# Optimization experiments

Hardware: AMD Instinct MI355X
Metric: run time of the kernel (lower is better)

Reference implementation:

```python
import jax, jax.numpy as jnp
import numpy as np

N = 25000      # nodes per type
E = 300000     # weight-edge rows
K = 16         # neighbors
F = 64         # in_feat
A = 64         # atten_dim
DW = 64        # weight_dim
CB = 8         # num_bit_conv
CV = 8         # num_vector_conv
OUT = 64       # out_feat
IN_K = CB * F + CV * (3 + 2 + 1)


def setup_inputs() -> dict:
    key = jax.random.key(0)
    ks = jax.random.split(key, 40)
    s = 0.05
    d = {}
    d['eu'] = jax.random.normal(ks[0], (N, F), jnp.float32)
    d['ei'] = jax.random.normal(ks[1], (N, F), jnp.float32)
    d['et'] = jax.random.normal(ks[2], (N, F), jnp.float32)
    d['ew'] = jax.random.normal(ks[3], (E, DW), jnp.float32)
    names = ['u_iw_j', 'u_tw_j', 'i_uw_j', 'i_tw_j', 't_uw_j', 't_iw_j']
    for i, nm in enumerate(names):
        d[nm] = jax.random.randint(ks[4 + i], (N, K), 0, N, jnp.int64 if jax.config.jax_enable_x64 else jnp.int32)
        d[nm.replace('_j', '_w')] = jax.random.randint(ks[10 + i], (N, K), 0, E, jnp.int64 if jax.config.jax_enable_x64 else jnp.int32)
    # per-type Attention1 params: user, item, tag
    for i, t in enumerate(['user', 'item', 'tag']):
        b = 16 + 4 * i
        d[f'W1_{t}'] = jax.random.normal(ks[b], (F + DW, A), jnp.float32) * s
        d[f'W2_{t}'] = jax.random.normal(ks[b + 1], (F, A), jnp.float32) * s
        d[f'b_{t}'] = jax.random.normal(ks[b + 2], (1, A), jnp.float32) * s
        d[f'v_{t}'] = jax.random.normal(ks[b + 3], (1, A), jnp.float32) * s
    d['U'] = jax.random.normal(ks[28], (F, A), jnp.float32) * s
    d['q'] = jax.random.normal(ks[29], (1, A), jnp.float32) * s
    d['p'] = jax.random.normal(ks[30], (1, A), jnp.float32) * s
    d['W_bit'] = jax.random.normal(ks[31], (CB, 3), jnp.float32) * s       # Conv2d(1,CB,(3,1))
    d['W_vec1'] = jax.random.normal(ks[32], (CV, 1, F), jnp.float32) * s   # Conv2d(1,CV,(1,F))
    d['W_vec2'] = jax.random.normal(ks[33], (CV, 2, F), jnp.float32) * s
    d['W_vec3'] = jax.random.normal(ks[34], (CV, 3, F), jnp.float32) * s
    d['Wf'] = jax.random.normal(ks[35], (IN_K, OUT), jnp.float32) * s
    d['bf'] = jax.random.normal(ks[36], (1, OUT), jnp.float32) * s
    return d


def _atten1(ev, ej, ew, v_j, v_w, W1, W2, b, v):
    ejp = jnp.concatenate([jnp.zeros((1, ej.shape[1]), ej.dtype), ej], axis=0)
    ewp = jnp.concatenate([jnp.zeros((1, ew.shape[1]), ew.dtype), ew], axis=0)
    eNj = ejp[v_j]                                  # [N,K,F]
    eNw = ewp[v_w]                                  # [N,K,DW]
    eNv = jnp.broadcast_to(ev[:, None, :], (ev.shape[0], v_j.shape[1], ev.shape[1]))
    eN_vw = jnp.concatenate([eNv, eNw], axis=-1)    # [N,K,F+DW]
    av = jnp.einsum('nkd,da->nka', eN_vw, W1) + jnp.einsum('nkf,fa->nka', eNj, W2) + b
    x = jax.nn.relu(av) @ v.T                       # [N,K,1]
    a = jax.nn.softmax(x, axis=1)
    return jnp.sum(a * eNj, axis=1)                 # [N,F]


def _atten2(u, i, t, U, q, p):
    uit = jnp.stack([u, i, t], axis=1)              # [N,3,F]
    x = jnp.einsum('nsf,fa->nsa', uit, U) + q
    x = jax.nn.relu(x) @ p.T                        # [N,3,1]
    b = jax.nn.softmax(x, axis=1)
    return b * uit                                  # [N,3,F]


def _conv(eN, W_bit, W_vec1, W_vec2, W_vec3):
    # eN: [N,3,F]
    bit = jax.nn.relu(jnp.einsum('njf,cj->ncf', eN, W_bit))       # [N,CB,F]
    bit = bit.reshape(bit.shape[0], -1)
    vec = []
    for j, W in ((1, W_vec1), (2, W_vec2), (3, W_vec3)):
        win = jnp.stack([eN[:, s:s + j, :] for s in range(3 - j + 1)], axis=1)  # [N,4-j,j,F]
        y = jax.nn.relu(jnp.einsum('nsjf,cjf->ncs', win, W))       # [N,CV,4-j]
        vec.append(y.reshape(y.shape[0], -1))
    return jnp.concatenate([bit] + vec, axis=1)                    # [N,IN_K]


def _forward(eu, ei, et, ew, params, idx):
    (W1u, W2u, bu, vu, W1i, W2i, bi, vi, W1t, W2t, bt, vt,
     U, q, p, W_bit, W_vec1, W_vec2, W_vec3, Wf, bf) = params
    (u_iw_j, u_iw_w, u_tw_j, u_tw_w, i_uw_j, i_uw_w,
     i_tw_j, i_tw_w, t_uw_j, t_uw_w, t_iw_j, t_iw_w) = idx
    eu_iN = _atten1(eu, ei, ew, u_iw_j, u_iw_w, W1i, W2i, bi, vi)
    eu_tN = _atten1(eu, et, ew, u_tw_j, u_tw_w, W1t, W2t, bt, vt)
    ei_uN = _atten1(ei, eu, ew, i_uw_j, i_uw_w, W1u, W2u, bu, vu)
    ei_tN = _atten1(ei, et, ew, i_tw_j, i_tw_w, W1t, W2t, bt, vt)
    et_uN = _atten1(et, eu, ew, t_uw_j, t_uw_w, W1u, W2u, bu, vu)
    et_iN = _atten1(et, ei, ew, t_iw_j, t_iw_w, W1i, W2i, bi, vi)
    euN = _atten2(eu, eu_iN, eu_tN, U, q, p)
    eiN = _atten2(ei_uN, ei, ei_tN, U, q, p)
    etN = _atten2(et_uN, et_iN, et, U, q, p)
    out = []
    for eN in (euN, eiN, etN):
        c = _conv(eN, W_bit, W_vec1, W_vec2, W_vec3)
        out.append(jax.nn.relu(c @ Wf + bf))
    return tuple(out)


def reference(eu, ei, et, ew,
              u_iw_j, u_iw_w, u_tw_j, u_tw_w, i_uw_j, i_uw_w, i_tw_j, i_tw_w,
              t_uw_j, t_uw_w, t_iw_j, t_iw_w,
              W1_user, W2_user, b_user, v_user,
              W1_item, W2_item, b_item, v_item,
              W1_tag, W2_tag, b_tag, v_tag,
              U, q, p, W_bit, W_vec1, W_vec2, W_vec3, Wf, bf):
    params = (W1_user, W2_user, b_user, v_user, W1_item, W2_item, b_item, v_item,
              W1_tag, W2_tag, b_tag, v_tag, U, q, p, W_bit, W_vec1, W_vec2, W_vec3, Wf, bf)
    idx = (u_iw_j, u_iw_w, u_tw_j, u_tw_w, i_uw_j, i_uw_w,
           i_tw_j, i_tw_w, t_uw_j, t_uw_w, t_iw_j, t_iw_w)
    return _forward(eu, ei, et, ew, params, idx)
```

## Files before the change

### kernel.cpp

```cpp
#include <hip/hip_runtime.h>
#include <math.h>

#define NN 25000
#define EE 300000
#define NT 1563
#define NT64 391
#define ET64 4688

typedef __attribute__((ext_vector_type(8))) short bf16x8;
typedef __attribute__((ext_vector_type(4))) float f32x4;
typedef __attribute__((ext_vector_type(2))) float f32x2;

__device__ __forceinline__ unsigned short f2bf(float f) {
    union { float f; unsigned u; } a; a.f = f;
    unsigned r = (a.u + 0x7fffu + ((a.u >> 16) & 1u)) >> 16;
    return (unsigned short)r;
}
__device__ __forceinline__ unsigned pack2(float lo, float hi) {
    return (unsigned)f2bf(lo) | ((unsigned)f2bf(hi) << 16);
}
__device__ __forceinline__ float bflo(unsigned p) {
    union { unsigned u; float f; } a; a.u = p << 16; return a.f;
}
__device__ __forceinline__ float bfhi(unsigned p) {
    union { unsigned u; float f; } a; a.u = p & 0xffff0000u; return a.f;
}
__device__ __forceinline__ unsigned packfp8x4(float a, float b, float c, float d) {
    int v = __builtin_amdgcn_cvt_pk_fp8_f32(a, b, 0, 0);
    v = __builtin_amdgcn_cvt_pk_fp8_f32(c, d, v, 1);
    return (unsigned)v;
}

__global__ __launch_bounds__(256) void head_kernel(
    const float* __restrict__ ew,
    const float* __restrict__ eu, const float* __restrict__ ei, const float* __restrict__ et,
    const float* __restrict__ W1u, const float* __restrict__ W1i, const float* __restrict__ W1t,
    const float* __restrict__ W2u, const float* __restrict__ W2i, const float* __restrict__ W2t,
    const float* __restrict__ bu, const float* __restrict__ bi, const float* __restrict__ bt,
    unsigned char* __restrict__ gw8, unsigned* __restrict__ preB,
    unsigned char* __restrict__ JG)
{
    __shared__ __align__(16) unsigned short stA[64 * 72];
    __shared__ __align__(16) float cS[64 * 68];
    const int t = threadIdx.x;
    const int lane = t & 63, wv = t >> 6;
    const int l15 = lane & 15, quad = lane >> 4;
    const int cw = wv * 16 + l15;
    const int bx = blockIdx.x;

    if (bx < ET64) {
        if (bx == 0 && t < 48) {
            int w = t >> 4;
            ((unsigned*)(gw8 + (size_t)w * (EE + 1) * 64))[t & 15] = 0u;
        }
        const float* Ws[3] = { W1u + 4096, W1i + 4096, W1t + 4096 };
        bf16x8 bf[3][2];
        #pragma unroll
        for (int w = 0; w < 3; ++w)
            #pragma unroll
            for (int ks = 0; ks < 2; ++ks)
                #pragma unroll
                for (int j = 0; j < 8; ++j)
                    bf[w][ks][j] = (short)f2bf(Ws[w][(ks * 32 + quad * 8 + j) * 64 + cw]);

        const int rowBase = bx * 64;
        #pragma unroll
        for (int i = 0; i < 4; ++i) {
            int idx = t + i * 256;
            int row = idx >> 4, cg = idx & 15;
            int gr = rowBase + row;
            float4 v4 = (gr < EE) ? *(const float4*)(ew + (size_t)gr * 64 + cg * 4)
                                  : make_float4(0.f, 0.f, 0.f, 0.f);
            uint2 pk = { pack2(v4.x, v4.y), pack2(v4.z, v4.w) };
            *(uint2*)&stA[row * 72 + cg * 4] = pk;
        }
        __syncthreads();
        bf16x8 af[4][2];
        #pragma unroll
        for (int m = 0; m < 4; ++m)
            #pragma unroll
            for (int ks = 0; ks < 2; ++ks)
                af[m][ks] = *(const bf16x8*)&stA[(m * 16 + l15) * 72 + ks * 32 + quad * 8];

        #pragma unroll
        for (int w = 0; w < 3; ++w) {
            if (w) __syncthreads();
            f32x4 acc[4];
            #pragma unroll
            for (int m = 0; m < 4; ++m) {
                acc[m].x = 0; acc[m].y = 0; acc[m].z = 0; acc[m].w = 0;
                #pragma unroll
                for (int ks = 0; ks < 2; ++ks)
                    acc[m] = __builtin_amdgcn_mfma_f32_16x16x32_bf16(af[m][ks], bf[w][ks], acc[m], 0, 0, 0);
                #pragma unroll
                for (int r = 0; r < 4; ++r)
                    cS[(m * 16 + quad * 4 + r) * 68 + cw] = acc[m][r];
            }
            __syncthreads();
            unsigned char* outg = gw8 + (size_t)w * (EE + 1) * 64 + 64;
            #pragma unroll
            for (int i = 0; i < 2; ++i) {
                int task = t + i * 256;
                int row = task >> 3, seg = task & 7;
                int gr = rowBase + row;
                if (gr < EE) {
                    float4 a = *(const float4*)&cS[row * 68 + seg * 8];
                    float4 b = *(const float4*)&cS[row * 68 + seg * 8 + 4];
                    uint2 pk = { packfp8x4(a.x, a.y, a.z, a.w),
                                 packfp8x4(b.x, b.y, b.z, b.w) };
                    *(uint2*)(outg + (size_t)gr * 64 + seg * 8) = pk;
                }
            }
        }
    } else {
        const int yy = bx - ET64;
        const int y = yy / NT64;
        const int rowBase = (yy - y * NT64) * 64;
        if (rowBase == 0 && t < 48)
            ((unsigned*)(JG + (size_t)y * (NN + 1) * 192))[t] = 0u;
        const float* X; const float* Wa; const float* Wb; const float* W2;
        const float* ba; const float* bb; int oa, ob;
        switch (y) {
            case 0:  X = eu; Wa = W1i; ba = bi; oa = 0; Wb = W1t; bb = bt; ob = 1; W2 = W2u; break;
            case 1:  X = ei; Wa = W1u; ba = bu; oa = 2; Wb = W1t; bb = bt; ob = 3; W2 = W2i; break;
            default: X = et; Wa = W1u; ba = bu; oa = 4; Wb = W1i; bb = bi; ob = 5; W2 = W2t; break;
        }
        const float* Ws[3] = { Wa, Wb, W2 };
        const float bias_cw[3] = { ba[cw], bb[cw], 0.f };
        bf16x8 bf[3][2];
        #pragma unroll
        for (int w = 0; w < 3; ++w)
            #pragma unroll
            for (int ks = 0; ks < 2; ++ks)
                #pragma unroll
                for (int j = 0; j < 8; ++j)
                    bf[w][ks][j] = (short)f2bf(Ws[w][(ks * 32 + quad * 8 + j) * 64 + cw]);

        #pragma unroll
        for (int i = 0; i < 4; ++i) {
            int idx = t + i * 256;
            int row = idx >> 4, cg = idx & 15;
            int gr = rowBase + row;
            float4 v4 = (gr < NN) ? *(const float4*)(X + (size_t)gr * 64 + cg * 4)
                                  : make_float4(0.f, 0.f, 0.f, 0.f);
            uint2 pk = { pack2(v4.x, v4.y), pack2(v4.z, v4.w) };
            *(uint2*)&stA[row * 72 + cg * 4] = pk;
        }
        __syncthreads();
        bf16x8 af[4][2];
        #pragma unroll
        for (int m = 0; m < 4; ++m)
            #pragma unroll
            for (int ks = 0; ks < 2; ++ks)
                af[m][ks] = *(const bf16x8*)&stA[(m * 16 + l15) * 72 + ks * 32 + quad * 8];

        #pragma unroll
        for (int w = 0; w < 3; ++w) {
            if (w) __syncthreads();
            f32x4 acc[4];
            #pragma unroll
            for (int m = 0; m < 4; ++m) {
                acc[m].x = 0; acc[m].y = 0; acc[m].z = 0; acc[m].w = 0;
                #pragma unroll
                for (int ks = 0; ks < 2; ++ks)
                    acc[m] = __builtin_amdgcn_mfma_f32_16x16x32_bf16(af[m][ks], bf[w][ks], acc[m], 0, 0, 0);
                #pragma unroll
                for (int r = 0; r < 4; ++r)
                    cS[(m * 16 + quad * 4 + r) * 68 + cw] = acc[m][r] + bias_cw[w];
            }
            __syncthreads();
            #pragma unroll
            for (int i = 0; i < 2; ++i) {
                int task = t + i * 256;
                int row = task >> 3, seg = task & 7;
                int gr = rowBase + row;
                if (gr >= NN) continue;
                float4 a = *(const float4*)&cS[row * 68 + seg * 8];
                float4 b = *(const float4*)&cS[row * 68 + seg * 8 + 4];
                if (w < 2) {
                    int oi = (w == 0) ? oa : ob;
                    uint4 pk = { pack2(a.x, a.y), pack2(a.z, a.w),
                                 pack2(b.x, b.y), pack2(b.z, b.w) };
                    *(uint4*)(preB + ((size_t)oi * NN + gr) * 32 + seg * 4) = pk;
                } else {
                    unsigned char* dst = JG + ((size_t)y * (NN + 1) + gr + 1) * 192;
                    uint2 gj = { packfp8x4(a.x, a.y, a.z, a.w),
                                 packfp8x4(b.x, b.y, b.z, b.w) };
                    *(uint2*)(dst + seg * 8) = gj;
                    uint4 ej = *(const uint4*)&stA[row * 72 + seg * 8];
                    *(uint4*)(dst + 64 + seg * 16) = ej;
                }
            }
        }
    }
}

__global__ __launch_bounds__(256) void atten1_kernel(
    const unsigned* __restrict__ preB, const unsigned char* __restrict__ gw8,
    const unsigned char* __restrict__ JG,
    const float* __restrict__ vu, const float* __restrict__ vi, const float* __restrict__ vt,
    const int* __restrict__ u_iw_j, const int* __restrict__ u_iw_w,
    const int* __restrict__ u_tw_j, const int* __restrict__ u_tw_w,
    const int* __restrict__ i_uw_j, const int* __restrict__ i_uw_w,
    const int* __restrict__ i_tw_j, const int* __restrict__ i_tw_w,
    const int* __restrict__ t_uw_j, const int* __restrict__ t_uw_w,
    const int* __restrict__ t_iw_j, const int* __restrict__ t_iw_w,
    unsigned* __restrict__ aoB)
{
    const int y = blockIdx.y;
    const int* Vj; const int* Vw; const float* v; int g;
    switch (y) {
        case 0:  Vj = u_iw_j; Vw = u_iw_w; v = vi; g = 1; break;
        case 1:  Vj = u_tw_j; Vw = u_tw_w; v = vt; g = 2; break;
        case 2:  Vj = i_uw_j; Vw = i_uw_w; v = vu; g = 0; break;
        case 3:  Vj = i_tw_j; Vw = i_tw_w; v = vt; g = 2; break;
        case 4:  Vj = t_uw_j; Vw = t_uw_w; v = vu; g = 0; break;
        default: Vj = t_iw_j; Vw = t_iw_w; v = vi; g = 1; break;
    }
    const unsigned* pre = preB + (size_t)y * NN * 32;
    const unsigned char* gw = gw8 + (size_t)g * (EE + 1) * 64;
    const unsigned char* jg = JG + (size_t)g * (NN + 1) * 192;
    unsigned*            out = aoB + (size_t)y * NN * 32;

    const int lane = threadIdx.x & 63;
    const int n = blockIdx.x * 4 + (threadIdx.x >> 6);
    const int q = lane >> 4, r = lane & 15;

    const uint2 prep = *(const uint2*)(pre + (size_t)n * 32 + 2 * r);
    const float pf0 = bflo(prep.x), pf1 = bfhi(prep.x);
    const float pf2 = bflo(prep.y), pf3 = bfhi(prep.y);
    const float4 v4 = *(const float4*)(v + r * 4);

    const int4 wi = *(const int4*)(Vw + n * 16 + q * 4);
    const int4 ji = *(const int4*)(Vj + n * 16 + q * 4);
    const int wid[4] = { wi.x, wi.y, wi.z, wi.w };
    const int jid[4] = { ji.x, ji.y, ji.z, ji.w };

    unsigned gwv[4], gjv[4]; uint2 ejv[4];
    #pragma unroll
    for (int i = 0; i < 4; ++i)
        gwv[i] = *(const unsigned*)(gw + (size_t)wid[i] * 64 + r * 4);
    #pragma unroll
    for (int i = 0; i < 4; ++i) {
        const unsigned char* row = jg + (size_t)jid[i] * 192;
        gjv[i] = *(const unsigned*)(row + r * 4);
        ejv[i] = *(const uint2*)(row + 64 + r * 8);
    }

    float xk[4];
    #pragma unroll
    for (int i = 0; i < 4; ++i) {
        f32x2 g01 = __builtin_amdgcn_cvt_pk_f32_fp8((int)gwv[i], false);
        f32x2 g23 = __builtin_amdgcn_cvt_pk_f32_fp8((int)gwv[i], true);
        f32x2 j01 = __builtin_amdgcn_cvt_pk_f32_fp8((int)gjv[i], false);
        f32x2 j23 = __builtin_amdgcn_cvt_pk_f32_fp8((int)gjv[i], true);
        float x =          fmaxf(pf0 + g01.x + j01.x, 0.f) * v4.x;
        x = fmaf(fmaxf(pf1 + g01.y + j01.y, 0.f), v4.y, x);
        x = fmaf(fmaxf(pf2 + g23.x + j23.x, 0.f), v4.z, x);
        x = fmaf(fmaxf(pf3 + g23.y + j23.y, 0.f), v4.w, x);
        x += __shfl_xor(x, 1, 64);
        x += __shfl_xor(x, 2, 64);
        x += __shfl_xor(x, 4, 64);
        x += __shfl_xor(x, 8, 64);
        xk[i] = x;
    }
    float m = fmaxf(fmaxf(xk[0], xk[1]), fmaxf(xk[2], xk[3]));
    m = fmaxf(m, __shfl_xor(m, 16, 64));
    m = fmaxf(m, __shfl_xor(m, 32, 64));
    float e0 = __expf(xk[0] - m), e1 = __expf(xk[1] - m);
    float e2 = __expf(xk[2] - m), e3 = __expf(xk[3] - m);
    float s = (e0 + e1) + (e2 + e3);
    s += __shfl_xor(s, 16, 64);
    s += __shfl_xor(s, 32, 64);
    const float inv = 1.f / s;

    float a0 = 0.f, a1 = 0.f, a2 = 0.f, a3 = 0.f;
    const float wgt[4] = { e0 * inv, e1 * inv, e2 * inv, e3 * inv };
    #pragma unroll
    for (int i = 0; i < 4; ++i) {
        a0 = fmaf(wgt[i], bflo(ejv[i].x), a0);
        a1 = fmaf(wgt[i], bfhi(ejv[i].x), a1);
        a2 = fmaf(wgt[i], bflo(ejv[i].y), a2);
        a3 = fmaf(wgt[i], bfhi(ejv[i].y), a3);
    }
    a0 += __shfl_xor(a0, 16, 64); a0 += __shfl_xor(a0, 32, 64);
    a1 += __shfl_xor(a1, 16, 64); a1 += __shfl_xor(a1, 32, 64);
    a2 += __shfl_xor(a2, 16, 64); a2 += __shfl_xor(a2, 32, 64);
    a3 += __shfl_xor(a3, 16, 64); a3 += __shfl_xor(a3, 32, 64);
    if (q == 0) {
        uint2 pk = { pack2(a0, a1), pack2(a2, a3) };
        *(uint2*)(out + (size_t)n * 32 + 2 * r) = pk;
    }
}

__global__ __launch_bounds__(256, 3) void tail_kernel(
    const float* __restrict__ eu, const float* __restrict__ ei, const float* __restrict__ et,
    const unsigned* __restrict__ aoB,
    const float* __restrict__ U, const float* __restrict__ q, const float* __restrict__ p,
    const float* __restrict__ Wbit, const float* __restrict__ Wv1,
    const float* __restrict__ Wv2, const float* __restrict__ Wv3,
    const float* __restrict__ Wf, const float* __restrict__ bfv,
    float* __restrict__ out)
{
    __shared__ __align__(16) unsigned short uitA[48 * 72];
    __shared__ __align__(16) unsigned short eNA[48 * 72];
    __shared__ __align__(16) unsigned short wcf[6 * 64 * 8];
    __shared__ __align__(16) unsigned short c_sh[16 * 584];
    __shared__ float G_sh[48 * 52];
    __shared__ float xpart[4 * 48];
    __shared__ float bcoef[16 * 4];

    const int t = threadIdx.x;
    const int lane = t & 63;
    const int wv = t >> 6;
    const int l15 = lane & 15;
    const int quad = lane >> 4;
    const int type = blockIdx.y;
    const float* xf = (type == 0) ? eu : (type == 1) ? ei : et;
    const int cw = wv * 16 + l15;
    const float qv = q[cw], pv = p[cw], bfb = bfv[cw];

    float wb[8][3];
    #pragma unroll
    for (int c = 0; c < 8; ++c)
        #pragma unroll
        for (int s = 0; s < 3; ++s) wb[c][s] = Wbit[c * 3 + s];

    bf16x8 ufrag[2];
    #pragma unroll
    for (int ks = 0; ks < 2; ++ks)
        #pragma unroll
        for (int j = 0; j < 8; ++j) {
            int f = ks * 32 + quad * 8 + j;
            ufrag[ks][j] = (short)f2bf(U[f * 64 + cw]);
        }
    bf16x8 wff[18];
    #pragma unroll
    for (int ks = 0; ks < 18; ++ks)
        #pragma unroll
        for (int j = 0; j < 8; ++j) {
            int k = ks * 32 + quad * 8 + j;
            float w = (k < 560) ? Wf[(size_t)k * 64 + cw] : 0.f;
            wff[ks][j] = (short)f2bf(w);
        }
    for (int slot = t; slot < 384; slot += 256) {
        int fi = slot >> 6, l = slot & 63;
        int nt_ = fi >> 1, ks = fi & 1;
        int r = nt_ * 16 + (l & 15);
        unsigned short vals[8];
        #pragma unroll
        for (int j = 0; j < 8; ++j) {
            int f = ks * 32 + (l >> 4) * 8 + j;
            float wv_;
            if (r < 8)       wv_ = Wv1[r * 64 + f];
            else if (r < 24) { int u = r - 8;  wv_ = Wv2[(u >> 1) * 128 + (u & 1) * 64 + f]; }
            else             { int u = r - 24; wv_ = Wv3[(u / 3) * 192 + (u % 3) * 64 + f]; }
            vals[j] = f2bf(wv_);
        }
        uint4 pk = { (unsigned)vals[0] | ((unsigned)vals[1] << 16),
                     (unsigned)vals[2] | ((unsigned)vals[3] << 16),
                     (unsigned)vals[4] | ((unsigned)vals[5] << 16),
                     (unsigned)vals[6] | ((unsigned)vals[7] << 16) };
        *(uint4*)&wcf[slot * 8] = pk;
    }

    for (int tile = blockIdx.x; tile < NT; tile += gridDim.x) {
        const int nodeBase = tile * 16;
        __syncthreads();
        #pragma unroll
        for (int i = 0; i < 3; ++i) {
            int idx = t + i * 256;
            int row = idx >> 4, cg = idx & 15;
            int nl = row / 3, s = row - nl * 3;
            int n = nodeBase + nl;
            uint2 pk;
            if (s == type) {
                float4 v4 = (n < NN) ? *(const float4*)(xf + (size_t)n * 64 + cg * 4)
                                     : make_float4(0.f, 0.f, 0.f, 0.f);
                pk.x = pack2(v4.x, v4.y); pk.y = pack2(v4.z, v4.w);
            } else {
                int aoidx = (type == 0) ? (s - 1)
                          : (type == 1) ? ((s == 0) ? 2 : 3)
                                        : ((s == 0) ? 4 : 5);
                pk = (n < NN) ? *(const uint2*)(aoB + ((size_t)aoidx * NN + n) * 32 + cg * 2)
                              : make_uint2(0u, 0u);
            }
            *(uint2*)&uitA[row * 72 + cg * 4] = pk;
        }
        __syncthreads();
        {
            f32x4 av[3];
            #pragma unroll
            for (int mt = 0; mt < 3; ++mt) { av[mt].x = 0; av[mt].y = 0; av[mt].z = 0; av[mt].w = 0; }
            #pragma unroll
            for (int mt = 0; mt < 3; ++mt)
                #pragma unroll
                for (int ks = 0; ks < 2; ++ks) {
                    bf16x8 a = *(const bf16x8*)&uitA[(mt * 16 + l15) * 72 + ks * 32 + quad * 8];
                    av[mt] = __builtin_amdgcn_mfma_f32_16x16x32_bf16(a, ufrag[ks], av[mt], 0, 0, 0);
                }
            #pragma unroll
            for (int mt = 0; mt < 3; ++mt)
                #pragma unroll
                for (int r = 0; r < 4; ++r) {
                    float val = fmaxf(av[mt][r] + qv, 0.f) * pv;
                    val += __shfl_xor(val, 1, 64); val += __shfl_xor(val, 2, 64);
                    val += __shfl_xor(val, 4, 64); val += __shfl_xor(val, 8, 64);
                    if (l15 == 0) xpart[wv * 48 + mt * 16 + quad * 4 + r] = val;
                }
        }
        __syncthreads();
        if (t < 16) {
            float xv[3];
            #pragma unroll
            for (int s = 0; s < 3; ++s)
                xv[s] = xpart[t * 3 + s] + xpart[48 + t * 3 + s]
                      + xpart[96 + t * 3 + s] + xpart[144 + t * 3 + s];
            float mm = fmaxf(xv[0], fmaxf(xv[1], xv[2]));
            float e0 = __expf(xv[0] - mm), e1 = __expf(xv[1] - mm), e2 = __expf(xv[2] - mm);
            float inv = 1.f / (e0 + e1 + e2);
            bcoef[t * 4 + 0] = e0 * inv; bcoef[t * 4 + 1] = e1 * inv; bcoef[t * 4 + 2] = e2 * inv;
        }
        __syncthreads();
        #pragma unroll
        for (int i = 0; i < 2; ++i) {
            int task = t + i * 256;
            int nl = task >> 5, fp = task & 31;
            float b0 = bcoef[nl * 4], b1 = bcoef[nl * 4 + 1], b2 = bcoef[nl * 4 + 2];
            unsigned u0 = *(const unsigned*)&uitA[(nl * 3 + 0) * 72 + fp * 2];
            unsigned u1 = *(const unsigned*)&uitA[(nl * 3 + 1) * 72 + fp * 2];
            unsigned u2 = *(const unsigned*)&uitA[(nl * 3 + 2) * 72 + fp * 2];
            float e0l = b0 * bflo(u0), e0h = b0 * bfhi(u0);
            float e1l = b1 * bflo(u1), e1h = b1 * bfhi(u1);
            float e2l = b2 * bflo(u2), e2h = b2 * bfhi(u2);
            *(unsigned*)&eNA[(nl * 3 + 0) * 72 + fp * 2] = pack2(e0l, e0h);
            *(unsigned*)&eNA[(nl * 3 + 1) * 72 + fp * 2] = pack2(e1l, e1h);
            *(unsigned*)&eNA[(nl * 3 + 2) * 72 + fp * 2] = pack2(e2l, e2h);
            #pragma unroll
            for (int c = 0; c < 8; ++c) {
                float lo = fmaxf(wb[c][0] * e0l + wb[c][1] * e1l + wb[c][2] * e2l, 0.f);
                float hi = fmaxf(wb[c][0] * e0h + wb[c][1] * e1h + wb[c][2] * e2h, 0.f);
                *(unsigned*)&c_sh[nl * 584 + c * 64 + fp * 2] = pack2(lo, hi);
            }
        }
        __syncthreads();
        #pragma unroll
        for (int pi = 0; pi < 3; ++pi) {
            int pr = wv + pi * 4;
            if (pr < 9) {
                int mm = pr / 3, nn_ = pr - mm * 3;
                f32x4 g; g.x = 0; g.y = 0; g.z = 0; g.w = 0;
                #pragma unroll
                for (int ks = 0; ks < 2; ++ks) {
                    bf16x8 a = *(const bf16x8*)&eNA[(mm * 16 + l15) * 72 + ks * 32 + quad * 8];
                    bf16x8 b = *(const bf16x8*)&wcf[((nn_ * 2 + ks) * 64 + lane) * 8];
                    g = __builtin_amdgcn_mfma_f32_16x16x32_bf16(a, b, g, 0, 0, 0);
                }
                #pragma unroll
                for (int r = 0; r < 4; ++r)
                    G_sh[(mm * 16 + quad * 4 + r) * 52 + nn_ * 16 + l15] = g[r];
            }
        }
        __syncthreads();
        #pragma unroll
        for (int i = 0; i < 4; ++i) {
            int task = t + i * 256;
            int vvv = task >> 4, nl = task & 15;
            unsigned short res = 0;
            if (vvv < 24) {
                int c = vvv / 3, s = vvv - c * 3;
                res = f2bf(fmaxf(G_sh[(nl * 3 + s) * 52 + c], 0.f));
            } else if (vvv < 40) {
                int u = vvv - 24, c = u >> 1, s = u & 1;
                float val = G_sh[(nl * 3 + s) * 52 + 8 + 2 * c]
                          + G_sh[(nl * 3 + s + 1) * 52 + 8 + 2 * c + 1];
                res = f2bf(fmaxf(val, 0.f));
            } else if (vvv < 48) {
                int c = vvv - 40;
                float val = G_sh[(nl * 3 + 0) * 52 + 24 + 3 * c]
                          + G_sh[(nl * 3 + 1) * 52 + 24 + 3 * c + 1]
                          + G_sh[(nl * 3 + 2) * 52 + 24 + 3 * c + 2];
                res = f2bf(fmaxf(val, 0.f));
            }
            c_sh[nl * 584 + 512 + vvv] = res;
        }
        __syncthreads();
        {
            f32x4 acc; acc.x = 0; acc.y = 0; acc.z = 0; acc.w = 0;
            const unsigned short* ap = &c_sh[l15 * 584 + quad * 8];
            #pragma unroll
            for (int ks = 0; ks < 18; ++ks) {
                bf16x8 a = *(const bf16x8*)(ap + ks * 32);
                acc = __builtin_amdgcn_mfma_f32_16x16x32_bf16(a, wff[ks], acc, 0, 0, 0);
            }
            float* outT = out + (size_t)type * NN * 64;
            #pragma unroll
            for (int r = 0; r < 4; ++r) {
                int node = nodeBase + quad * 4 + r;
                if (node < NN) outT[(size_t)node * 64 + cw] = fmaxf(acc[r] + bfb, 0.f);
            }
        }
    }
}

extern "C" void kernel_launch(void* const* d_in, const int* in_sizes, int n_in,
                              void* d_out, int out_size, void* d_ws, size_t ws_size,
                              hipStream_t stream)
{
    const float* eu = (const float*)d_in[0];
    const float* ei = (const float*)d_in[1];
    const float* et = (const float*)d_in[2];
    const float* ew = (const float*)d_in[3];
    const int* u_iw_j = (const int*)d_in[4];
    const int* u_iw_w = (const int*)d_in[5];
    const int* u_tw_j = (const int*)d_in[6];
    const int* u_tw_w = (const int*)d_in[7];
    const int* i_uw_j = (const int*)d_in[8];
    const int* i_uw_w = (const int*)d_in[9];
    const int* i_tw_j = (const int*)d_in[10];
    const int* i_tw_w = (const int*)d_in[11];
    const int* t_uw_j = (const int*)d_in[12];
    const int* t_uw_w = (const int*)d_in[13];
    const int* t_iw_j = (const int*)d_in[14];
    const int* t_iw_w = (const int*)d_in[15];
    const float* W1_user = (const float*)d_in[16];
    const float* W2_user = (const float*)d_in[17];
    const float* b_user  = (const float*)d_in[18];
    const float* v_user  = (const float*)d_in[19];
    const float* W1_item = (const float*)d_in[20];
    const float* W2_item = (const float*)d_in[21];
    const float* b_item  = (const float*)d_in[22];
    const float* v_item  = (const float*)d_in[23];
    const float* W1_tag  = (const float*)d_in[24];
    const float* W2_tag  = (const float*)d_in[25];
    const float* b_tag   = (const float*)d_in[26];
    const float* v_tag   = (const float*)d_in[27];
    const float* U    = (const float*)d_in[28];
    const float* q    = (const float*)d_in[29];
    const float* p    = (const float*)d_in[30];
    const float* Wbit = (const float*)d_in[31];
    const float* Wv1  = (const float*)d_in[32];
    const float* Wv2  = (const float*)d_in[33];
    const float* Wv3  = (const float*)d_in[34];
    const float* Wf   = (const float*)d_in[35];
    const float* bfv  = (const float*)d_in[36];
    float* out = (float*)d_out;

    unsigned char* gw8 = (unsigned char*)d_ws;
    unsigned* preB = (unsigned*)(gw8 + (size_t)3 * (EE + 1) * 64);
    unsigned char* JG = (unsigned char*)(preB + (size_t)6 * NN * 32);
    unsigned* aoB = (unsigned*)(JG + (size_t)3 * (NN + 1) * 192);

    const dim3 blk(256);

    head_kernel<<<ET64 + 3 * NT64, blk, 0, stream>>>(
        ew, eu, ei, et,
        W1_user, W1_item, W1_tag, W2_user, W2_item, W2_tag,
        b_user, b_item, b_tag, gw8, preB, JG);

    atten1_kernel<<<dim3(NN / 4, 6), blk, 0, stream>>>(
        preB, gw8, JG, v_user, v_item, v_tag,
        u_iw_j, u_iw_w, u_tw_j, u_tw_w, i_uw_j, i_uw_w,
        i_tw_j, i_tw_w, t_uw_j, t_uw_w, t_iw_j, t_iw_w, aoB);

    tail_kernel<<<dim3(256, 3), blk, 0, stream>>>(
        eu, ei, et, aoB,
        U, q, p, Wbit, Wv1, Wv2, Wv3, Wf, bfv, out);
}
```

Before: 401.0 us.

## Use packed fp16 math in atten1 scoring and group blocks by gather table

The preB projection is now stored as fp16 instead of bf16. The atten1 score computation converts fp8 directly to packed half, adds and relus in packed fp16, and accumulates with fdot2 instead of scalar fp32 FMAs. The launch grid is also reordered so that adjacent blocks gather from the same embedding/weight table (by type g), which is meant to improve L2 locality for the random gathers. fp16 accumulation of the sums adds some precision risk.

```diff
diff --git a/kernel.cpp b/kernel.cpp
--- a/kernel.cpp
+++ b/kernel.cpp
@@ -10,6 +10,7 @@
 typedef __attribute__((ext_vector_type(8))) short bf16x8;
 typedef __attribute__((ext_vector_type(4))) float f32x4;
 typedef __attribute__((ext_vector_type(2))) float f32x2;
+typedef __attribute__((ext_vector_type(2))) __fp16 h2;
 
 __device__ __forceinline__ unsigned short f2bf(float f) {
     union { float f; unsigned u; } a; a.f = f;
@@ -29,6 +30,37 @@
     int v = __builtin_amdgcn_cvt_pk_fp8_f32(a, b, 0, 0);
     v = __builtin_amdgcn_cvt_pk_fp8_f32(c, d, v, 1);
     return (unsigned)v;
+}
+__device__ __forceinline__ unsigned pkh(float lo, float hi) {
+    h2 r = __builtin_amdgcn_cvt_pkrtz(lo, hi);
+    return __builtin_bit_cast(unsigned, r);
+}
+template<bool HI>
+__device__ __forceinline__ h2 fp8toh(unsigned v) {
+#if __has_builtin(__builtin_amdgcn_cvt_scalef32_pk_f16_fp8)
+    return __builtin_amdgcn_cvt_scalef32_pk_f16_fp8((int)v, 1.0f, HI);
+#else
+    f32x2 f = __builtin_amdgcn_cvt_pk_f32_fp8((int)v, HI);
+    return __builtin_amdgcn_cvt_pkrtz(f.x, f.y);
+#endif
+}
+__device__ __forceinline__ float hdot(h2 a, h2 b, float c) {
+#if __has_builtin(__builtin_amdgcn_fdot2)
+    return __builtin_amdgcn_fdot2(a, b, c, false);
+#else
+    return c + (float)a[0] * (float)b[0] + (float)a[1] * (float)b[1];
+#endif
+}
+__device__ __forceinline__ h2 hmax0(h2 a) {
+    h2 z; z[0] = (__fp16)0.f; z[1] = (__fp16)0.f;
+#if __has_builtin(__builtin_elementwise_max)
+    return __builtin_elementwise_max(a, z);
+#else
+    h2 r;
+    r[0] = a[0] > z[0] ? a[0] : z[0];
+    r[1] = a[1] > z[1] ? a[1] : z[1];
+    return r;
+#endif
 }
 
 __global__ __launch_bounds__(256) void head_kernel(
@@ -179,8 +211,8 @@
                 float4 b = *(const float4*)&cS[row * 68 + seg * 8 + 4];
                 if (w < 2) {
                     int oi = (w == 0) ? oa : ob;
-                    uint4 pk = { pack2(a.x, a.y), pack2(a.z, a.w),
-                                 pack2(b.x, b.y), pack2(b.z, b.w) };
+                    uint4 pk = { pkh(a.x, a.y), pkh(a.z, a.w),
+                                 pkh(b.x, b.y), pkh(b.z, b.w) };
                     *(uint4*)(preB + ((size_t)oi * NN + gr) * 32 + seg * 4) = pk;
                 } else {
                     unsigned char* dst = JG + ((size_t)y * (NN + 1) + gr + 1) * 192;
@@ -207,29 +239,34 @@
     const int* __restrict__ t_iw_j, const int* __restrict__ t_iw_w,
     unsigned* __restrict__ aoB)
 {
-    const int y = blockIdx.y;
-    const int* Vj; const int* Vw; const float* v; int g;
-    switch (y) {
-        case 0:  Vj = u_iw_j; Vw = u_iw_w; v = vi; g = 1; break;
-        case 1:  Vj = u_tw_j; Vw = u_tw_w; v = vt; g = 2; break;
-        case 2:  Vj = i_uw_j; Vw = i_uw_w; v = vu; g = 0; break;
-        case 3:  Vj = i_tw_j; Vw = i_tw_w; v = vt; g = 2; break;
-        case 4:  Vj = t_uw_j; Vw = t_uw_w; v = vu; g = 0; break;
-        default: Vj = t_iw_j; Vw = t_iw_w; v = vi; g = 1; break;
-    }
+    const int g = blockIdx.y;
+    const int p = blockIdx.x & 1;
+    const int tile = blockIdx.x >> 1;
+    int y; const int* Vj; const int* Vw;
+    switch (g * 2 + p) {
+        case 0:  y = 2; Vj = i_uw_j; Vw = i_uw_w; break;
+        case 1:  y = 4; Vj = t_uw_j; Vw = t_uw_w; break;
+        case 2:  y = 0; Vj = u_iw_j; Vw = u_iw_w; break;
+        case 3:  y = 5; Vj = t_iw_j; Vw = t_iw_w; break;
+        case 4:  y = 1; Vj = u_tw_j; Vw = u_tw_w; break;
+        default: y = 3; Vj = i_tw_j; Vw = i_tw_w; break;
+    }
+    const float* v = (g == 0) ? vu : (g == 1) ? vi : vt;
     const unsigned* pre = preB + (size_t)y * NN * 32;
     const unsigned char* gw = gw8 + (size_t)g * (EE + 1) * 64;
     const unsigned char* jg = JG + (size_t)g * (NN + 1) * 192;
     unsigned*            out = aoB + (size_t)y * NN * 32;
 
     const int lane = threadIdx.x & 63;
-    const int n = blockIdx.x * 4 + (threadIdx.x >> 6);
+    const int n = tile * 4 + (threadIdx.x >> 6);
     const int q = lane >> 4, r = lane & 15;
 
     const uint2 prep = *(const uint2*)(pre + (size_t)n * 32 + 2 * r);
-    const float pf0 = bflo(prep.x), pf1 = bfhi(prep.x);
-    const float pf2 = bflo(prep.y), pf3 = bfhi(prep.y);
+    const h2 pre01 = __builtin_bit_cast(h2, prep.x);
+    const h2 pre23 = __builtin_bit_cast(h2, prep.y);
     const float4 v4 = *(const float4*)(v + r * 4);
+    const h2 v01h = __builtin_amdgcn_cvt_pkrtz(v4.x, v4.y);
+    const h2 v23h = __builtin_amdgcn_cvt_pkrtz(v4.z, v4.w);
 
     const int4 wi = *(const int4*)(Vw + n * 16 + q * 4);
     const int4 ji = *(const int4*)(Vj + n * 16 + q * 4);
@@ -250,14 +287,14 @@
     float xk[4];
     #pragma unroll
     for (int i = 0; i < 4; ++i) {
-        f32x2 g01 = __builtin_amdgcn_cvt_pk_f32_fp8((int)gwv[i], false);
-        f32x2 g23 = __builtin_amdgcn_cvt_pk_f32_fp8((int)gwv[i], true);
-        f32x2 j01 = __builtin_amdgcn_cvt_pk_f32_fp8((int)gjv[i], false);
-        f32x2 j23 = __builtin_amdgcn_cvt_pk_f32_fp8((int)gjv[i], true);
-        float x =          fmaxf(pf0 + g01.x + j01.x, 0.f) * v4.x;
-        x = fmaf(fmaxf(pf1 + g01.y + j01.y, 0.f), v4.y, x);
-        x = fmaf(fmaxf(pf2 + g23.x + j23.x, 0.f), v4.z, x);
-        x = fmaf(fmaxf(pf3 + g23.y + j23.y, 0.f), v4.w, x);
+        h2 g01 = fp8toh<false>(gwv[i]);
+        h2 g23 = fp8toh<true>(gwv[i]);
+        h2 j01 = fp8toh<false>(gjv[i]);
+        h2 j23 = fp8toh<true>(gjv[i]);
+        h2 z01 = hmax0(pre01 + g01 + j01);
+        h2 z23 = hmax0(pre23 + g23 + j23);
+        float x = hdot(z01, v01h, 0.f);
+        x = hdot(z23, v23h, x);
         x += __shfl_xor(x, 1, 64);
         x += __shfl_xor(x, 2, 64);
         x += __shfl_xor(x, 4, 64);
@@ -558,7 +595,7 @@
         W1_user, W1_item, W1_tag, W2_user, W2_item, W2_tag,
         b_user, b_item, b_tag, gw8, preB, JG);
 
-    atten1_kernel<<<dim3(NN / 4, 6), blk, 0, stream>>>(
+    atten1_kernel<<<dim3(2 * (NN / 4), 3), blk, 0, stream>>>(
         preB, gw8, JG, v_user, v_item, v_tag,
         u_iw_j, u_iw_w, u_tw_j, u_tw_w, i_uw_j, i_uw_w,
         i_tw_j, i_tw_w, t_uw_j, t_uw_w, t_iw_j, t_iw_w, aoB);
```

New measurement: 396.0 us. Within noise of the previous version (-1.2%).
